# Kernel tuning notes

Measured on AMD Instinct MI355X. Metric: run time of the kernel, lower is better.

Reference implementation:

```python
import jax, jax.numpy as jnp
import numpy as np

N, E, F, H, L, G, C = 50000, 800000, 64, 128, 4, 64, 10
GAMMA = 10.0  # Gaussian RBF width for centers in (0,1)
CENTERS = jnp.linspace(0.0, 1.0, H)


def _ssp(v):
    # shifted softplus, SchNet's nonlinearity
    return jax.nn.softplus(v) - 0.6931472


def setup_inputs() -> dict:
    key = jax.random.key(0)
    ks = jax.random.split(key, 20)

    def w(k, shape, fan_in):
        return (jax.random.normal(k, shape, dtype=jnp.float32) / np.sqrt(fan_in)).astype(jnp.float32)

    x = jax.random.normal(ks[0], (N, F), dtype=jnp.float32)
    edge_dist = jax.random.uniform(ks[1], (E,), dtype=jnp.float32)
    edge_src = jax.random.randint(ks[2], (E,), 0, N, dtype=jnp.int32)
    edge_dst = jax.random.randint(ks[3], (E,), 0, N, dtype=jnp.int32)
    graph_ids = jnp.sort(jax.random.randint(ks[4], (N,), 0, G, dtype=jnp.int32))

    return {
        "x": x, "edge_dist": edge_dist,
        "edge_src": edge_src, "edge_dst": edge_dst, "graph_ids": graph_ids,
        # first-layer node projection F->H, remaining layers H->H (stacked)
        "W1_0": w(ks[5], (F, H), F), "b1_0": jnp.zeros((H,), jnp.float32),
        "W1_rest": w(ks[6], (L - 1, H, H), H), "b1_rest": jnp.zeros((L - 1, H), jnp.float32),
        # filter-generating MLP on RBF features, per layer
        "Wf1": w(ks[7], (L, H, H), H), "bf1": jnp.zeros((L, H), jnp.float32),
        "Wf2": w(ks[8], (L, H, H), H), "bf2": jnp.zeros((L, H), jnp.float32),
        # output projection per layer
        "W2": w(ks[9], (L, H, H), H), "b2": jnp.zeros((L, H), jnp.float32),
        # readout FC
        "fc_w": w(ks[10], (H, C), H), "fc_b": jnp.zeros((C,), jnp.float32),
    }


def _schnet_conv(x, rbf, src, dst, W1, b1, Wf1, bf1, Wf2, bf2, W2, b2):
    # CFConv: project nodes, gate gathered source features with a distance
    # filter, scatter-sum to destinations, project out.
    filt = _ssp(rbf @ Wf1 + bf1) @ Wf2 + bf2          # [E, H]
    h = x @ W1 + b1                                    # [N, H]
    msg = h[src] * filt                                # [E, H] gather + gate
    agg = jax.ops.segment_sum(msg, dst, num_segments=N)  # [N, H] scatter-sum
    return agg @ W2 + b2


def reference(x, edge_dist, edge_src, edge_dst, graph_ids,
              W1_0, b1_0, W1_rest, b1_rest, Wf1, bf1, Wf2, bf2, W2, b2,
              fc_w, fc_b):
    # Gaussian radial basis expansion of edge distances, shared across layers
    rbf = jnp.exp(-GAMMA * (edge_dist[:, None] - CENTERS) ** 2)  # [E, H]

    h = jax.nn.relu(_schnet_conv(x, rbf, edge_src, edge_dst,
                                 W1_0, b1_0, Wf1[0], bf1[0], Wf2[0], bf2[0],
                                 W2[0], b2[0]))
    for i in range(L - 1):
        h = jax.nn.relu(_schnet_conv(h, rbf, edge_src, edge_dst,
                                     W1_rest[i], b1_rest[i],
                                     Wf1[i + 1], bf1[i + 1],
                                     Wf2[i + 1], bf2[i + 1],
                                     W2[i + 1], b2[i + 1]))

    # dgl.mean_nodes: per-graph mean over nodes
    sums = jax.ops.segment_sum(h, graph_ids, num_segments=G)           # [G, H]
    cnts = jax.ops.segment_sum(jnp.ones((N,), h.dtype), graph_ids, num_segments=G)
    pooled = sums / jnp.maximum(cnts, 1.0)[:, None]

    logits = pooled @ fc_w + fc_b                                       # [G, C]
    return jax.nn.log_softmax(logits, axis=1)
```

## Files before the change

kernel.cpp:

```cpp
#include <hip/hip_runtime.h>
#include <math.h>

#define NN 50000
#define EE 800000
#define FF 64
#define HH 128
#define LL 4
#define GG 64
#define CC 10
#define TT 512
#define BD 64
#define ABLK 1024
#define EPB 782
#define SEGC 192
#define SUBB 96
#define SRW 6250

#define PB_CVTW 8
#define PB_TAB ((TT / 16) * LL)
#define PB_CVTX (NN * FF / 4 / 256)
#define PB_PART ABLK

#define SCB (8 * SUBB)
#define GEMMB (NN / 16)

typedef unsigned short ushort_t;
typedef unsigned int uint_t;

typedef short s8v __attribute__((ext_vector_type(8)));
typedef float f32x4 __attribute__((ext_vector_type(4)));

__device__ inline ushort_t f2bf(float f) {
  uint_t u = __float_as_uint(f);
  uint_t r = (u + 0x7FFFu + ((u >> 16) & 1u)) >> 16;
  return (ushort_t)r;
}
__device__ inline float bf_lo(uint_t pair) { return __uint_as_float(pair << 16); }
__device__ inline float bf_hi(uint_t pair) { return __uint_as_float(pair & 0xFFFF0000u); }
__device__ inline float bf1f(ushort_t v) { return __uint_as_float(((uint_t)v) << 16); }

__global__ __launch_bounds__(256) void prep(
    const float* __restrict__ x, ushort_t* __restrict__ xb,
    const float* __restrict__ W1_0, const float* __restrict__ W1_rest,
    const float* __restrict__ W2, ushort_t* __restrict__ wt,
    const float* __restrict__ Wf1, const float* __restrict__ bf1,
    const float* __restrict__ Wf2, const float* __restrict__ bf2,
    ushort_t* __restrict__ tables,
    const int* __restrict__ dst, const int* __restrict__ src,
    const float* __restrict__ dist,
    uint2* __restrict__ seg, int* __restrict__ segcnt, int* __restrict__ bcnt,
    const int* __restrict__ gid, int* __restrict__ gcnt, float* __restrict__ gsum) {
  __shared__ float rbf[16][HH];
  __shared__ float hid[16][HH];
  __shared__ int lcnt[8];
  int tid = threadIdx.x;
  int b = blockIdx.x;

  if (b < PB_CVTW) {
    int mid = b;
    const float* srcm; int K;
    if (mid == 0) { srcm = W1_0; K = FF; }
    else if (mid < 4) { srcm = W1_rest + (size_t)(mid - 1) * HH * HH; K = HH; }
    else { srcm = W2 + (size_t)(mid - 4) * HH * HH; K = HH; }
    ushort_t* dstm = wt + (size_t)mid * HH * HH;
    for (int idx = tid; idx < K * HH; idx += 256) {
      int k = idx >> 7, n = idx & 127;
      dstm[n * K + k] = f2bf(srcm[idx]);
    }
  } else if (b < PB_CVTW + PB_TAB) {
    int bb = b - PB_CVTW;
    int l = bb & 3;
    int tb = (bb >> 2) * 16;
    int j = tid & 127;
    float c = j * (1.0f / (HH - 1));
#pragma unroll
    for (int tt2 = 0; tt2 < 16; ++tt2) {
      float d = (tb + tt2) * (1.0f / (TT - 1));
      float dd = d - c;
      rbf[tt2][j] = expf(-10.0f * dd * dd);
    }
    __syncthreads();
    const float* W1f = Wf1 + (size_t)l * HH * HH;
    float s[16];
    float bb1 = bf1[l * HH + j];
#pragma unroll
    for (int tt2 = 0; tt2 < 16; ++tt2) s[tt2] = bb1;
    for (int k = 0; k < HH; ++k) {
      float wk = W1f[(size_t)k * HH + j];
#pragma unroll
      for (int tt2 = 0; tt2 < 16; ++tt2) s[tt2] += rbf[tt2][k] * wk;
    }
#pragma unroll
    for (int tt2 = 0; tt2 < 16; ++tt2)
      hid[tt2][j] = fmaxf(s[tt2], 0.f) + log1pf(expf(-fabsf(s[tt2]))) - 0.6931472f;
    __syncthreads();
    const float* W2f = Wf2 + (size_t)l * HH * HH;
    float bb2 = bf2[l * HH + j];
#pragma unroll
    for (int tt2 = 0; tt2 < 16; ++tt2) s[tt2] = bb2;
    for (int k = 0; k < HH; ++k) {
      float wk = W2f[(size_t)k * HH + j];
#pragma unroll
      for (int tt2 = 0; tt2 < 16; ++tt2) s[tt2] += hid[tt2][k] * wk;
    }
    if (tid < 128) {
#pragma unroll
      for (int tt2 = 0; tt2 < 16; ++tt2)
        tables[((size_t)l * TT + tb + tt2) * HH + j] = f2bf(s[tt2]);
    }
  } else if (b < PB_CVTW + PB_TAB + PB_CVTX) {
    int i = (b - PB_CVTW - PB_TAB) * 256 + tid;
    const float4* x4 = (const float4*)x;
    float4 v = x4[i];
    union { ushort_t us[4]; uint2 u; } pk;
    pk.us[0] = f2bf(v.x); pk.us[1] = f2bf(v.y); pk.us[2] = f2bf(v.z); pk.us[3] = f2bf(v.w);
    *(uint2*)&xb[i * 4] = pk.u;
  } else if (b < PB_CVTW + PB_TAB + PB_CVTX + PB_PART) {
    int pb = b - PB_CVTW - PB_TAB - PB_CVTX;
    if (tid < 8) lcnt[tid] = 0;
    int z = pb * 49 + tid;
    if (tid < 49 && z < NN) bcnt[z] = 0;
    __syncthreads();
    int e0 = pb * EPB;
    int e1 = min(e0 + EPB, EE);
    for (int e = e0 + tid; e < e1; e += 256) {
      int d = __builtin_nontemporal_load(dst + e);
      int s = __builtin_nontemporal_load(src + e);
      float di = __builtin_nontemporal_load(dist + e);
      float u = di * (float)(TT - 1);
      int t0 = (int)(fminf(fmaxf(u, 0.f), (float)(TT - 1)) + 0.5f);
      if (t0 > TT - 1) t0 = TT - 1;
      int r = d / SRW;
      int pos = atomicAdd(&lcnt[r], 1);
      if (pos < SEGC)
        seg[((size_t)(r << 10) + pb) * SEGC + pos] =
            make_uint2((uint_t)d, ((uint_t)s << 9) | (uint_t)t0);
    }
    __syncthreads();
    if (tid < 8) segcnt[(tid << 10) + pb] = min(lcnt[tid], SEGC);
  } else {
    for (int i = tid; i < GG * HH; i += 256) gsum[i] = 0.f;
    if (tid < GG) {
      int g = tid;
      int lo = 0, hi = NN;
      while (lo < hi) { int m = (lo + hi) >> 1; if (gid[m] < g) lo = m + 1; else hi = m; }
      int b0 = lo;
      lo = 0; hi = NN;
      int g1 = g + 1;
      while (lo < hi) { int m = (lo + hi) >> 1; if (gid[m] < g1) lo = m + 1; else hi = m; }
      gcnt[g] = lo - b0;
    }
  }
}

__global__ __launch_bounds__(256) void scatter_gemm1(
    const uint2* __restrict__ seg, const int* __restrict__ segcnt,
    int* __restrict__ bcnt, uint_t* __restrict__ epad,
    const ushort_t* __restrict__ xb, const ushort_t* __restrict__ wt,
    const float* __restrict__ b1_0, ushort_t* __restrict__ pbuf) {
  int tid = threadIdx.x;
  if (blockIdx.x < SCB) {
    int r = blockIdx.x & 7;
    int sub = blockIdx.x >> 3;
    for (int b = sub; b < ABLK; b += SUBB) {
      int cnt = segcnt[(r << 10) + b];
      const uint_t* sp = (const uint_t*)(seg + ((size_t)(r << 10) + b) * SEGC);
      for (int i = tid; i < cnt; i += 256) {
        uint_t ex = __builtin_nontemporal_load(sp + i * 2);
        uint_t ey = __builtin_nontemporal_load(sp + i * 2 + 1);
        int slot = atomicAdd(&bcnt[ex], 1);
        if (slot < BD) epad[(size_t)ex * BD + slot] = ey;
      }
    }
  } else {
    int tile = blockIdx.x - SCB;
    int lane = tid & 63, wave = tid >> 6, m = lane & 15, quad = lane >> 4;
    int rowbase = tile * 16, colbase = wave * 32;
    const ushort_t* arow = xb + (size_t)(rowbase + m) * FF;
    const ushort_t* brow0 = wt + (size_t)(colbase + m) * FF;
    const ushort_t* brow1 = wt + (size_t)(colbase + 16 + m) * FF;
    f32x4 acc0 = {0.f, 0.f, 0.f, 0.f};
    f32x4 acc1 = {0.f, 0.f, 0.f, 0.f};
    for (int kc = 0; kc < FF; kc += 32) {
      int k = kc + quad * 8;
      union { uint4 u; s8v v; } a, b0, b1;
      a.u  = *(const uint4*)(arow + k);
      b0.u = *(const uint4*)(brow0 + k);
      b1.u = *(const uint4*)(brow1 + k);
      acc0 = __builtin_amdgcn_mfma_f32_16x16x32_bf16(a.v, b0.v, acc0, 0, 0, 0);
      acc1 = __builtin_amdgcn_mfma_f32_16x16x32_bf16(a.v, b1.v, acc1, 0, 0, 0);
    }
    float bb0 = b1_0[colbase + m];
    float bb1 = b1_0[colbase + 16 + m];
#pragma unroll
    for (int reg = 0; reg < 4; ++reg) {
      int row = rowbase + quad * 4 + reg;
      pbuf[(size_t)row * HH + colbase + m] = f2bf(acc0[reg] + bb0);
      pbuf[(size_t)row * HH + colbase + 16 + m] = f2bf(acc1[reg] + bb1);
    }
  }
}

__global__ __launch_bounds__(256) void fused_layer(
    const ushort_t* __restrict__ pIn, const ushort_t* __restrict__ table,
    const uint_t* __restrict__ epad, const int* __restrict__ bcnt,
    const ushort_t* __restrict__ WT2, const float* __restrict__ b2l,
    const ushort_t* __restrict__ WT1, const float* __restrict__ b1l,
    ushort_t* __restrict__ OUT, int last) {
  __shared__ ushort_t At[16 * 128];
  __shared__ ushort_t T[16 * 128];
  int tid = threadIdx.x;
  int lane = tid & 63;
  int wv = tid >> 6;
  int tile = blockIdx.x;
#pragma unroll
  for (int i = 0; i < 4; ++i) {
    int r = wv * 4 + i;
    int v = tile * 16 + r;
    int n = min(bcnt[v], BD);
    uint_t ed = (lane < n) ? epad[(size_t)v * BD + lane] : 0u;
    float ax = 0.f, ay = 0.f;
    int j = 0;
    int n8 = n & ~7;
    for (; j < n8; j += 8) {
      uint_t e0 = __shfl(ed, j + 0), e1 = __shfl(ed, j + 1);
      uint_t e2 = __shfl(ed, j + 2), e3 = __shfl(ed, j + 3);
      uint_t e4 = __shfl(ed, j + 4), e5 = __shfl(ed, j + 5);
      uint_t e6 = __shfl(ed, j + 6), e7 = __shfl(ed, j + 7);
      uint_t pv0 = ((const uint_t*)(pIn + (size_t)(e0 >> 9) * HH))[lane];
      uint_t pv1 = ((const uint_t*)(pIn + (size_t)(e1 >> 9) * HH))[lane];
      uint_t pv2 = ((const uint_t*)(pIn + (size_t)(e2 >> 9) * HH))[lane];
      uint_t pv3 = ((const uint_t*)(pIn + (size_t)(e3 >> 9) * HH))[lane];
      uint_t pv4 = ((const uint_t*)(pIn + (size_t)(e4 >> 9) * HH))[lane];
      uint_t pv5 = ((const uint_t*)(pIn + (size_t)(e5 >> 9) * HH))[lane];
      uint_t pv6 = ((const uint_t*)(pIn + (size_t)(e6 >> 9) * HH))[lane];
      uint_t pv7 = ((const uint_t*)(pIn + (size_t)(e7 >> 9) * HH))[lane];
      uint_t f0 = ((const uint_t*)(table + (size_t)(e0 & 511u) * HH))[lane];
      uint_t f1 = ((const uint_t*)(table + (size_t)(e1 & 511u) * HH))[lane];
      uint_t f2 = ((const uint_t*)(table + (size_t)(e2 & 511u) * HH))[lane];
      uint_t f3 = ((const uint_t*)(table + (size_t)(e3 & 511u) * HH))[lane];
      uint_t f4 = ((const uint_t*)(table + (size_t)(e4 & 511u) * HH))[lane];
      uint_t f5 = ((const uint_t*)(table + (size_t)(e5 & 511u) * HH))[lane];
      uint_t f6 = ((const uint_t*)(table + (size_t)(e6 & 511u) * HH))[lane];
      uint_t f7 = ((const uint_t*)(table + (size_t)(e7 & 511u) * HH))[lane];
      ax += bf_lo(pv0) * bf_lo(f0); ay += bf_hi(pv0) * bf_hi(f0);
      ax += bf_lo(pv1) * bf_lo(f1); ay += bf_hi(pv1) * bf_hi(f1);
      ax += bf_lo(pv2) * bf_lo(f2); ay += bf_hi(pv2) * bf_hi(f2);
      ax += bf_lo(pv3) * bf_lo(f3); ay += bf_hi(pv3) * bf_hi(f3);
      ax += bf_lo(pv4) * bf_lo(f4); ay += bf_hi(pv4) * bf_hi(f4);
      ax += bf_lo(pv5) * bf_lo(f5); ay += bf_hi(pv5) * bf_hi(f5);
      ax += bf_lo(pv6) * bf_lo(f6); ay += bf_hi(pv6) * bf_hi(f6);
      ax += bf_lo(pv7) * bf_lo(f7); ay += bf_hi(pv7) * bf_hi(f7);
    }
    if (n - j >= 4) {
      uint_t e0 = __shfl(ed, j + 0), e1 = __shfl(ed, j + 1);
      uint_t e2 = __shfl(ed, j + 2), e3 = __shfl(ed, j + 3);
      uint_t pv0 = ((const uint_t*)(pIn + (size_t)(e0 >> 9) * HH))[lane];
      uint_t pv1 = ((const uint_t*)(pIn + (size_t)(e1 >> 9) * HH))[lane];
      uint_t pv2 = ((const uint_t*)(pIn + (size_t)(e2 >> 9) * HH))[lane];
      uint_t pv3 = ((const uint_t*)(pIn + (size_t)(e3 >> 9) * HH))[lane];
      uint_t f0 = ((const uint_t*)(table + (size_t)(e0 & 511u) * HH))[lane];
      uint_t f1 = ((const uint_t*)(table + (size_t)(e1 & 511u) * HH))[lane];
      uint_t f2 = ((const uint_t*)(table + (size_t)(e2 & 511u) * HH))[lane];
      uint_t f3 = ((const uint_t*)(table + (size_t)(e3 & 511u) * HH))[lane];
      ax += bf_lo(pv0) * bf_lo(f0); ay += bf_hi(pv0) * bf_hi(f0);
      ax += bf_lo(pv1) * bf_lo(f1); ay += bf_hi(pv1) * bf_hi(f1);
      ax += bf_lo(pv2) * bf_lo(f2); ay += bf_hi(pv2) * bf_hi(f2);
      ax += bf_lo(pv3) * bf_lo(f3); ay += bf_hi(pv3) * bf_hi(f3);
      j += 4;
    }
    for (; j < n; ++j) {
      uint_t e = __shfl(ed, j);
      uint_t pv = ((const uint_t*)(pIn + (size_t)(e >> 9) * HH))[lane];
      uint_t f = ((const uint_t*)(table + (size_t)(e & 511u) * HH))[lane];
      ax += bf_lo(pv) * bf_lo(f);
      ay += bf_hi(pv) * bf_hi(f);
    }
    uint_t packed = (uint_t)f2bf(ax) | ((uint_t)f2bf(ay) << 16);
    ((uint_t*)At)[r * 64 + (((lane >> 2) ^ r) << 2) + (lane & 3)] = packed;
  }
  __syncthreads();
  int m = lane & 15, quad = lane >> 4;
  int rowbase = tile * 16, colbase = wv * 32;
  {
    const ushort_t* brow0 = WT2 + (size_t)(colbase + m) * HH;
    const ushort_t* brow1 = WT2 + (size_t)(colbase + 16 + m) * HH;
    f32x4 acc0 = {0.f, 0.f, 0.f, 0.f};
    f32x4 acc1 = {0.f, 0.f, 0.f, 0.f};
    for (int kc = 0; kc < HH; kc += 32) {
      int k = kc + quad * 8;
      int g = k >> 3;
      union { uint4 u; s8v v; } a, b0, b1;
      a.u = *(const uint4*)&At[m * 128 + ((g ^ m) << 3)];
      b0.u = *(const uint4*)(brow0 + k);
      b1.u = *(const uint4*)(brow1 + k);
      acc0 = __builtin_amdgcn_mfma_f32_16x16x32_bf16(a.v, b0.v, acc0, 0, 0, 0);
      acc1 = __builtin_amdgcn_mfma_f32_16x16x32_bf16(a.v, b1.v, acc1, 0, 0, 0);
    }
    float bb0 = b2l[colbase + m];
    float bb1 = b2l[colbase + 16 + m];
    if (last) {
#pragma unroll
      for (int reg = 0; reg < 4; ++reg) {
        int row = rowbase + quad * 4 + reg;
        OUT[(size_t)row * HH + colbase + m] = f2bf(fmaxf(acc0[reg] + bb0, 0.f));
        OUT[(size_t)row * HH + colbase + 16 + m] = f2bf(fmaxf(acc1[reg] + bb1, 0.f));
      }
      return;
    }
#pragma unroll
    for (int reg = 0; reg < 4; ++reg) {
      int r = quad * 4 + reg;
      float v0 = fmaxf(acc0[reg] + bb0, 0.f);
      float v1 = fmaxf(acc1[reg] + bb1, 0.f);
      int c0 = colbase + m, c1 = colbase + 16 + m;
      T[r * 128 + (((c0 >> 3) ^ r) << 3) + (c0 & 7)] = f2bf(v0);
      T[r * 128 + (((c1 >> 3) ^ r) << 3) + (c1 & 7)] = f2bf(v1);
    }
  }
  __syncthreads();
  {
    const ushort_t* brow0 = WT1 + (size_t)(colbase + m) * HH;
    const ushort_t* brow1 = WT1 + (size_t)(colbase + 16 + m) * HH;
    f32x4 acc0 = {0.f, 0.f, 0.f, 0.f};
    f32x4 acc1 = {0.f, 0.f, 0.f, 0.f};
    for (int kc = 0; kc < HH; kc += 32) {
      int k0 = kc + quad * 8;
      int g = k0 >> 3;
      union { uint4 u; s8v v; } a, b0, b1;
      a.u = *(const uint4*)&T[m * 128 + ((g ^ m) << 3)];
      b0.u = *(const uint4*)(brow0 + k0);
      b1.u = *(const uint4*)(brow1 + k0);
      acc0 = __builtin_amdgcn_mfma_f32_16x16x32_bf16(a.v, b0.v, acc0, 0, 0, 0);
      acc1 = __builtin_amdgcn_mfma_f32_16x16x32_bf16(a.v, b1.v, acc1, 0, 0, 0);
    }
    float bb0 = b1l[colbase + m];
    float bb1 = b1l[colbase + 16 + m];
#pragma unroll
    for (int reg = 0; reg < 4; ++reg) {
      int row = rowbase + quad * 4 + reg;
      OUT[(size_t)row * HH + colbase + m] = f2bf(acc0[reg] + bb0);
      OUT[(size_t)row * HH + colbase + 16 + m] = f2bf(acc1[reg] + bb1);
    }
  }
}

__global__ __launch_bounds__(128) void pool_kernel(const ushort_t* __restrict__ h, const int* __restrict__ gid,
                                                   float* __restrict__ gsum) {
  int j = threadIdx.x;
  int i0 = blockIdx.x * 128;
  int i1 = min(i0 + 128, NN);
  if (i0 >= NN) return;
  float acc = 0.f;
  int gcur = gid[i0];
  for (int i = i0; i < i1; ++i) {
    int g = gid[i];
    if (g != gcur) {
      atomicAdd(&gsum[gcur * HH + j], acc);
      acc = 0.f;
      gcur = g;
    }
    acc += bf1f(h[(size_t)i * HH + j]);
  }
  atomicAdd(&gsum[gcur * HH + j], acc);
}

__global__ __launch_bounds__(128) void final_kernel(const float* __restrict__ gsum, const int* __restrict__ gcnt,
                                                    const float* __restrict__ fc_w, const float* __restrict__ fc_b,
                                                    float* __restrict__ out) {
  int g = blockIdx.x, j = threadIdx.x;
  __shared__ float pooled[HH];
  __shared__ float logits[CC];
  __shared__ float lse;
  float cnt = fmaxf((float)gcnt[g], 1.0f);
  pooled[j] = gsum[g * HH + j] / cnt;
  __syncthreads();
  if (j < CC) {
    float s = fc_b[j];
    for (int k = 0; k < HH; ++k) s += pooled[k] * fc_w[k * CC + j];
    logits[j] = s;
  }
  __syncthreads();
  if (j == 0) {
    float m = -1e30f;
    for (int c = 0; c < CC; ++c) m = fmaxf(m, logits[c]);
    float s = 0.f;
    for (int c = 0; c < CC; ++c) s += expf(logits[c] - m);
    lse = m + logf(s);
  }
  __syncthreads();
  if (j < CC) out[g * CC + j] = logits[j] - lse;
}

extern "C" void kernel_launch(void* const* d_in, const int* in_sizes, int n_in,
                              void* d_out, int out_size, void* d_ws, size_t ws_size,
                              hipStream_t stream) {
  const float* x       = (const float*)d_in[0];
  const float* edist   = (const float*)d_in[1];
  const int*   esrc    = (const int*)d_in[2];
  const int*   edst    = (const int*)d_in[3];
  const int*   gid     = (const int*)d_in[4];
  const float* W1_0    = (const float*)d_in[5];
  const float* b1_0    = (const float*)d_in[6];
  const float* W1_rest = (const float*)d_in[7];
  const float* b1_rest = (const float*)d_in[8];
  const float* Wf1     = (const float*)d_in[9];
  const float* bf1     = (const float*)d_in[10];
  const float* Wf2     = (const float*)d_in[11];
  const float* bf2     = (const float*)d_in[12];
  const float* W2      = (const float*)d_in[13];
  const float* b2      = (const float*)d_in[14];
  const float* fc_w    = (const float*)d_in[15];
  const float* fc_b    = (const float*)d_in[16];
  float* out = (float*)d_out;

  char* ws = (char*)d_ws;
  size_t o = 0;
  auto alloc = [&](size_t bytes) {
    void* p = ws + o;
    o += (bytes + 255) & ~(size_t)255;
    return p;
  };
  ushort_t* tables = (ushort_t*)alloc(sizeof(ushort_t) * (size_t)LL * TT * HH);
  ushort_t* xb     = (ushort_t*)alloc(sizeof(ushort_t) * (size_t)NN * FF);
  ushort_t* wt     = (ushort_t*)alloc(sizeof(ushort_t) * 8 * HH * HH);
  ushort_t* pbuf   = (ushort_t*)alloc(sizeof(ushort_t) * (size_t)NN * HH);
  ushort_t* pbuf2  = (ushort_t*)alloc(sizeof(ushort_t) * (size_t)NN * HH);
  ushort_t* hbuf   = (ushort_t*)alloc(sizeof(ushort_t) * (size_t)NN * HH);
  int*      bcnt   = (int*)alloc(sizeof(int) * NN);
  uint_t*   epad   = (uint_t*)alloc(sizeof(uint_t) * (size_t)NN * BD);
  uint2*    seg    = (uint2*)alloc(sizeof(uint2) * (size_t)8 * ABLK * SEGC);
  int*      segcnt = (int*)alloc(sizeof(int) * 8 * ABLK);
  float*    gsum   = (float*)alloc(sizeof(float) * GG * HH);
  int*      gcnt   = (int*)alloc(sizeof(int) * GG);

  const int prepBlocks = PB_CVTW + PB_TAB + PB_CVTX + PB_PART + 1;
  prep<<<prepBlocks, 256, 0, stream>>>(x, xb, W1_0, W1_rest, W2, wt,
                                       Wf1, bf1, Wf2, bf2, tables,
                                       edst, esrc, edist, seg, segcnt, bcnt,
                                       gid, gcnt, gsum);
  scatter_gemm1<<<SCB + GEMMB, 256, 0, stream>>>(seg, segcnt, bcnt, epad,
                                                 xb, wt, b1_0, pbuf);

  ushort_t* pIn = pbuf;
  ushort_t* pOut = pbuf2;
  for (int l = 0; l < LL; ++l) {
    int last = (l == LL - 1);
    fused_layer<<<GEMMB, 256, 0, stream>>>(
        pIn, tables + (size_t)l * TT * HH, epad, bcnt,
        wt + (size_t)(4 + l) * HH * HH, b2 + (size_t)l * HH,
        last ? nullptr : (wt + (size_t)(1 + l) * HH * HH),
        last ? nullptr : (b1_rest + (size_t)l * HH),
        last ? hbuf : pOut, last);
    ushort_t* tmp = pIn; pIn = pOut; pOut = tmp;
  }

  pool_kernel<<<(NN + 127) / 128, 128, 0, stream>>>(hbuf, gid, gsum);
  final_kernel<<<GG, 128, 0, stream>>>(gsum, gcnt, fc_w, fc_b, out);
}
```

Before: 403.5 us.

## Interleave gather across four nodes per wave using zero filter row padding

The filter table gets a zero row at index 0, and edge codes now carry a 1-based table index, so an empty padded edge slot contributes nothing. The per-wave aggregation then walks four destination nodes together in batches of four edges using readlane instead of shuffles, with no per-node tail loops. This gives more independent loads in flight and removes branching, at the cost of wasted loads for nodes with fewer edges than the wave's maximum. Source indices shift to 10 bits of table code, which still fits 50000 nodes.

Result: no change. 405.9 us (+0.6%).

```diff
diff --git a/kernel.cpp b/kernel.cpp
--- a/kernel.cpp
+++ b/kernel.cpp
@@ -9,6 +9,7 @@
 #define GG 64
 #define CC 10
 #define TT 512
+#define TTP 513
 #define BD 64
 #define ABLK 1024
 #define EPB 782
@@ -106,7 +107,7 @@
     if (tid < 128) {
 #pragma unroll
       for (int tt2 = 0; tt2 < 16; ++tt2)
-        tables[((size_t)l * TT + tb + tt2) * HH + j] = f2bf(s[tt2]);
+        tables[((size_t)l * TTP + 1 + tb + tt2) * HH + j] = f2bf(s[tt2]);
     }
   } else if (b < PB_CVTW + PB_TAB + PB_CVTX) {
     int i = (b - PB_CVTW - PB_TAB) * 256 + tid;
@@ -134,12 +135,14 @@
       int pos = atomicAdd(&lcnt[r], 1);
       if (pos < SEGC)
         seg[((size_t)(r << 10) + pb) * SEGC + pos] =
-            make_uint2((uint_t)d, ((uint_t)s << 9) | (uint_t)t0);
+            make_uint2((uint_t)d, ((uint_t)s << 10) | (uint_t)(t0 + 1));
     }
     __syncthreads();
     if (tid < 8) segcnt[(tid << 10) + pb] = min(lcnt[tid], SEGC);
   } else {
     for (int i = tid; i < GG * HH; i += 256) gsum[i] = 0.f;
+    for (int i = tid; i < LL * HH; i += 256)
+      tables[(size_t)(i >> 7) * TTP * HH + (i & 127)] = 0;
     if (tid < GG) {
       int g = tid;
       int lo = 0, hi = NN;
@@ -213,70 +216,39 @@
   int lane = tid & 63;
   int wv = tid >> 6;
   int tile = blockIdx.x;
+  const uint_t* pu = (const uint_t*)pIn;
+  const uint_t* tu = (const uint_t*)table;
+
+  int baseV = tile * 16 + wv * 4;
+  uint_t ed[4];
+  float ax[4], ay[4];
+  int B = 0;
+#pragma unroll
+  for (int i = 0; i < 4; ++i) {
+    int n = min(bcnt[baseV + i], BD);
+    ed[i] = (lane < n) ? epad[(size_t)(baseV + i) * BD + lane] : 0u;
+    int nb = (n + 3) >> 2;
+    B = max(B, nb);
+    ax[i] = 0.f; ay[i] = 0.f;
+  }
+  for (int b = 0; b < B; ++b) {
+    int j4 = b << 2;
+#pragma unroll
+    for (int i = 0; i < 4; ++i) {
+#pragma unroll
+      for (int k = 0; k < 4; ++k) {
+        uint_t e = (uint_t)__builtin_amdgcn_readlane((int)ed[i], j4 + k);
+        uint_t pv = pu[(size_t)(e >> 10) * 64 + lane];
+        uint_t fv = tu[(size_t)(e & 1023u) * 64 + lane];
+        ax[i] += bf_lo(pv) * bf_lo(fv);
+        ay[i] += bf_hi(pv) * bf_hi(fv);
+      }
+    }
+  }
 #pragma unroll
   for (int i = 0; i < 4; ++i) {
     int r = wv * 4 + i;
-    int v = tile * 16 + r;
-    int n = min(bcnt[v], BD);
-    uint_t ed = (lane < n) ? epad[(size_t)v * BD + lane] : 0u;
-    float ax = 0.f, ay = 0.f;
-    int j = 0;
-    int n8 = n & ~7;
-    for (; j < n8; j += 8) {
-      uint_t e0 = __shfl(ed, j + 0), e1 = __shfl(ed, j + 1);
-      uint_t e2 = __shfl(ed, j + 2), e3 = __shfl(ed, j + 3);
-      uint_t e4 = __shfl(ed, j + 4), e5 = __shfl(ed, j + 5);
-      uint_t e6 = __shfl(ed, j + 6), e7 = __shfl(ed, j + 7);
-      uint_t pv0 = ((const uint_t*)(pIn + (size_t)(e0 >> 9) * HH))[lane];
-      uint_t pv1 = ((const uint_t*)(pIn + (size_t)(e1 >> 9) * HH))[lane];
-      uint_t pv2 = ((const uint_t*)(pIn + (size_t)(e2 >> 9) * HH))[lane];
-      uint_t pv3 = ((const uint_t*)(pIn + (size_t)(e3 >> 9) * HH))[lane];
-      uint_t pv4 = ((const uint_t*)(pIn + (size_t)(e4 >> 9) * HH))[lane];
-      uint_t pv5 = ((const uint_t*)(pIn + (size_t)(e5 >> 9) * HH))[lane];
-      uint_t pv6 = ((const uint_t*)(pIn + (size_t)(e6 >> 9) * HH))[lane];
-      uint_t pv7 = ((const uint_t*)(pIn + (size_t)(e7 >> 9) * HH))[lane];
-      uint_t f0 = ((const uint_t*)(table + (size_t)(e0 & 511u) * HH))[lane];
-      uint_t f1 = ((const uint_t*)(table + (size_t)(e1 & 511u) * HH))[lane];
-      uint_t f2 = ((const uint_t*)(table + (size_t)(e2 & 511u) * HH))[lane];
-      uint_t f3 = ((const uint_t*)(table + (size_t)(e3 & 511u) * HH))[lane];
-      uint_t f4 = ((const uint_t*)(table + (size_t)(e4 & 511u) * HH))[lane];
-      uint_t f5 = ((const uint_t*)(table + (size_t)(e5 & 511u) * HH))[lane];
-      uint_t f6 = ((const uint_t*)(table + (size_t)(e6 & 511u) * HH))[lane];
-      uint_t f7 = ((const uint_t*)(table + (size_t)(e7 & 511u) * HH))[lane];
-      ax += bf_lo(pv0) * bf_lo(f0); ay += bf_hi(pv0) * bf_hi(f0);
-      ax += bf_lo(pv1) * bf_lo(f1); ay += bf_hi(pv1) * bf_hi(f1);
-      ax += bf_lo(pv2) * bf_lo(f2); ay += bf_hi(pv2) * bf_hi(f2);
-      ax += bf_lo(pv3) * bf_lo(f3); ay += bf_hi(pv3) * bf_hi(f3);
-      ax += bf_lo(pv4) * bf_lo(f4); ay += bf_hi(pv4) * bf_hi(f4);
-      ax += bf_lo(pv5) * bf_lo(f5); ay += bf_hi(pv5) * bf_hi(f5);
-      ax += bf_lo(pv6) * bf_lo(f6); ay += bf_hi(pv6) * bf_hi(f6);
-      ax += bf_lo(pv7) * bf_lo(f7); ay += bf_hi(pv7) * bf_hi(f7);
-    }
-    if (n - j >= 4) {
-      uint_t e0 = __shfl(ed, j + 0), e1 = __shfl(ed, j + 1);
-      uint_t e2 = __shfl(ed, j + 2), e3 = __shfl(ed, j + 3);
-      uint_t pv0 = ((const uint_t*)(pIn + (size_t)(e0 >> 9) * HH))[lane];
-      uint_t pv1 = ((const uint_t*)(pIn + (size_t)(e1 >> 9) * HH))[lane];
-      uint_t pv2 = ((const uint_t*)(pIn + (size_t)(e2 >> 9) * HH))[lane];
-      uint_t pv3 = ((const uint_t*)(pIn + (size_t)(e3 >> 9) * HH))[lane];
-      uint_t f0 = ((const uint_t*)(table + (size_t)(e0 & 511u) * HH))[lane];
-      uint_t f1 = ((const uint_t*)(table + (size_t)(e1 & 511u) * HH))[lane];
-      uint_t f2 = ((const uint_t*)(table + (size_t)(e2 & 511u) * HH))[lane];
-      uint_t f3 = ((const uint_t*)(table + (size_t)(e3 & 511u) * HH))[lane];
-      ax += bf_lo(pv0) * bf_lo(f0); ay += bf_hi(pv0) * bf_hi(f0);
-      ax += bf_lo(pv1) * bf_lo(f1); ay += bf_hi(pv1) * bf_hi(f1);
-      ax += bf_lo(pv2) * bf_lo(f2); ay += bf_hi(pv2) * bf_hi(f2);
-      ax += bf_lo(pv3) * bf_lo(f3); ay += bf_hi(pv3) * bf_hi(f3);
-      j += 4;
-    }
-    for (; j < n; ++j) {
-      uint_t e = __shfl(ed, j);
-      uint_t pv = ((const uint_t*)(pIn + (size_t)(e >> 9) * HH))[lane];
-      uint_t f = ((const uint_t*)(table + (size_t)(e & 511u) * HH))[lane];
-      ax += bf_lo(pv) * bf_lo(f);
-      ay += bf_hi(pv) * bf_hi(f);
-    }
-    uint_t packed = (uint_t)f2bf(ax) | ((uint_t)f2bf(ay) << 16);
+    uint_t packed = (uint_t)f2bf(ax[i]) | ((uint_t)f2bf(ay[i]) << 16);
     ((uint_t*)At)[r * 64 + (((lane >> 2) ^ r) << 2) + (lane & 3)] = packed;
   }
   __syncthreads();
@@ -421,7 +393,7 @@
     o += (bytes + 255) & ~(size_t)255;
     return p;
   };
-  ushort_t* tables = (ushort_t*)alloc(sizeof(ushort_t) * (size_t)LL * TT * HH);
+  ushort_t* tables = (ushort_t*)alloc(sizeof(ushort_t) * (size_t)LL * TTP * HH);
   ushort_t* xb     = (ushort_t*)alloc(sizeof(ushort_t) * (size_t)NN * FF);
   ushort_t* wt     = (ushort_t*)alloc(sizeof(ushort_t) * 8 * HH * HH);
   ushort_t* pbuf   = (ushort_t*)alloc(sizeof(ushort_t) * (size_t)NN * HH);
@@ -447,7 +419,7 @@
   for (int l = 0; l < LL; ++l) {
     int last = (l == LL - 1);
     fused_layer<<<GEMMB, 256, 0, stream>>>(
-        pIn, tables + (size_t)l * TT * HH, epad, bcnt,
+        pIn, tables + (size_t)l * TTP * HH, epad, bcnt,
         wt + (size_t)(4 + l) * HH * HH, b2 + (size_t)l * HH,
         last ? nullptr : (wt + (size_t)(1 + l) * HH * HH),
         last ? nullptr : (b1_rest + (size_t)l * HH),
```
